# Optimization experiments

Hardware: AMD Instinct MI355X
Metric: run time of the kernel (lower is better)

Reference implementation:

```python
import jax, jax.numpy as jnp
import numpy as np

HEADS = 8
DIM_HEAD = 64
SCALE = DIM_HEAD ** -0.5


def setup_inputs() -> dict:
    key = jax.random.key(0)
    ks = jax.random.split(key, 6)
    B, T, C, H, W = 16, 64, 512, 64, 64
    inner = HEADS * DIM_HEAD  # 512
    return {
        "vision_feature": jax.random.normal(ks[0], (B, C, H, W), jnp.float32),
        "language_feature": jax.random.normal(ks[1], (B, T, C), jnp.float32),
        "mask": jnp.ones((B, T), jnp.int32),  # unused by the module's forward
        "Wq": jax.random.normal(ks[2], (inner, C), jnp.float32) * (C ** -0.5),
        "Wk": jax.random.normal(ks[3], (inner, C), jnp.float32) * (C ** -0.5),
        "Wv": jax.random.normal(ks[4], (inner, C), jnp.float32) * (C ** -0.5),
        "Wo": jax.random.normal(ks[5], (C, inner), jnp.float32) * (inner ** -0.5),
    }


def reference(vision_feature, language_feature, mask, Wq, Wk, Wv, Wo):
    B, T, C = language_feature.shape
    _, _, H, W = vision_feature.shape
    S = H * W
    # 1x1 conv projections == matmuls over the channel dim
    q = jnp.einsum('btc,ic->bti', language_feature, Wq)           # (B, T, inner)
    vis = vision_feature.reshape(B, C, S)                          # (B, C, S)
    k = jnp.einsum('ic,bcs->bis', Wk, vis)                         # (B, inner, S)
    v = jnp.einsum('ic,bcs->bis', Wv, vis)                         # (B, inner, S)
    # split heads: channel index = n*dim_head + d  (n outermost)
    q = q.reshape(B, T, HEADS, DIM_HEAD).transpose(2, 0, 1, 3)     # (h, B, T, d)
    k = k.reshape(B, HEADS, DIM_HEAD, S).transpose(1, 0, 2, 3)     # (h, B, d, S)
    v = v.reshape(B, HEADS, DIM_HEAD, S).transpose(1, 0, 3, 2)     # (h, B, S, d)
    att = jax.nn.softmax(jnp.einsum('hbtd,hbds->hbts', q, k) * SCALE, axis=-1)
    out = jnp.einsum('hbts,hbsd->hbtd', att, v)                    # (h, B, T, d)
    # merge heads back: b (n c) tokens -> equivalently (B, T, h*d)
    out = out.transpose(1, 2, 0, 3).reshape(B, T, HEADS * DIM_HEAD)
    out = jnp.einsum('bti,oi->bto', out, Wo)                       # (B, T, C)
    return out
```

## Files before the change

### kernel.cpp

```cpp
#include <hip/hip_runtime.h>
#include <stdint.h>

typedef __attribute__((ext_vector_type(8))) short short8;
typedef __attribute__((ext_vector_type(4))) short short4v;
typedef __attribute__((ext_vector_type(4))) float float4v;
typedef __attribute__((ext_vector_type(8))) __bf16 bf16x8;

#define NCH 4

__device__ __forceinline__ float4v mfma16x16x32(short8 a, short8 b, float4v c) {
  return __builtin_amdgcn_mfma_f32_16x16x32_bf16(
      __builtin_bit_cast(bf16x8, a), __builtin_bit_cast(bf16x8, b), c, 0, 0, 0);
}

__device__ __forceinline__ short f2bf(float f) {
  uint32_t u = __builtin_bit_cast(uint32_t, f);
  u += 0x7fffu + ((u >> 16) & 1u);
  return (short)(u >> 16);
}

__device__ __forceinline__ float bf2f(short s) {
  return __builtin_bit_cast(float, ((uint32_t)(uint16_t)s) << 16);
}

__device__ __forceinline__ void load_lds16(const short* g, short* l) {
  __builtin_amdgcn_global_load_lds(
      (const __attribute__((address_space(1))) void*)g,
      (__attribute__((address_space(3))) void*)l, 16, 0, 0);
}

__global__ __launch_bounds__(256) void convert5(
    const float* __restrict__ sl, short* __restrict__ dl,
    const float* __restrict__ s1, short* __restrict__ d1,
    const float* __restrict__ s2, short* __restrict__ d2,
    const float* __restrict__ s3, short* __restrict__ d3,
    const float* __restrict__ s4, short* __restrict__ d4) {
  const float* src; short* dst; int n4;
  switch (blockIdx.y) {
    case 0: src = sl; dst = dl; n4 = 131072; break;
    case 1: src = s1; dst = d1; n4 = 65536; break;
    case 2: src = s2; dst = d2; n4 = 65536; break;
    case 3: src = s3; dst = d3; n4 = 65536; break;
    default: src = s4; dst = d4; n4 = 65536; break;
  }
  const int stride = gridDim.x * blockDim.x;
  for (int i = blockIdx.x * blockDim.x + threadIdx.x; i < n4; i += stride) {
    float4v v = *(const float4v*)(src + (long)i * 4);
    short4v o;
#pragma unroll
    for (int r = 0; r < 4; r++) o[r] = f2bf(v[r]);
    *(short4v*)(dst + (long)i * 4) = o;
  }
}

template <int OUT_F32>
__global__ __launch_bounds__(256) void gemm_nt(
    const short* __restrict__ A, const short* __restrict__ B,
    void* __restrict__ C, int K, int ldc, float scale) {
  __shared__ alignas(16) short lA[128 * 32];
  __shared__ alignas(16) short lB[128 * 32];
  const int tid = threadIdx.x;
  const int lane = tid & 63, w = tid >> 6;
  const int quad = lane >> 4, l16 = lane & 15;
  const int wm = w >> 1, wn = w & 1;
  const long m0 = (long)blockIdx.y * 128, n0 = (long)blockIdx.x * 128;

  float4v acc[4][4];
#pragma unroll
  for (int i = 0; i < 4; i++)
#pragma unroll
    for (int j = 0; j < 4; j++) acc[i][j] = (float4v)0.0f;

  const int srow = tid >> 2;
  const int scol = (((tid & 3) ^ ((srow >> 1) & 3))) * 8;

  load_lds16(&A[(m0 + srow) * K + scol], &lA[tid * 8]);
  load_lds16(&A[(m0 + 64 + srow) * K + scol], &lA[2048 + tid * 8]);
  load_lds16(&B[(n0 + srow) * K + scol], &lB[tid * 8]);
  load_lds16(&B[(n0 + 64 + srow) * K + scol], &lB[2048 + tid * 8]);

  for (int kt = 0; kt < K; kt += 32) {
    __syncthreads();

    short8 af[4], bf[4];
#pragma unroll
    for (int t = 0; t < 4; t++) {
      const int ra = wm * 64 + t * 16 + l16;
      const int rb = wn * 64 + t * 16 + l16;
      af[t] = *(const short8*)&lA[ra * 32 + ((quad ^ ((ra >> 1) & 3)) * 8)];
      bf[t] = *(const short8*)&lB[rb * 32 + ((quad ^ ((rb >> 1) & 3)) * 8)];
    }
    __syncthreads();

    if (kt + 32 < K) {
      load_lds16(&A[(m0 + srow) * K + kt + 32 + scol], &lA[tid * 8]);
      load_lds16(&A[(m0 + 64 + srow) * K + kt + 32 + scol], &lA[2048 + tid * 8]);
      load_lds16(&B[(n0 + srow) * K + kt + 32 + scol], &lB[tid * 8]);
      load_lds16(&B[(n0 + 64 + srow) * K + kt + 32 + scol], &lB[2048 + tid * 8]);
    }
#pragma unroll
    for (int i = 0; i < 4; i++)
#pragma unroll
      for (int j = 0; j < 4; j++)
        acc[i][j] = mfma16x16x32(af[i], bf[j], acc[i][j]);
  }

  const int cm = wm * 64 + quad * 4;
  const int cn = wn * 64 + l16;
  if (OUT_F32) {
    float* Cf = (float*)C;
#pragma unroll
    for (int i = 0; i < 4; i++)
#pragma unroll
      for (int j = 0; j < 4; j++) {
        const long gn = n0 + cn + j * 16;
#pragma unroll
        for (int r = 0; r < 4; r++)
          Cf[(m0 + cm + i * 16 + r) * (long)ldc + gn] = acc[i][j][r] * scale;
      }
  } else {
    short* Cs = (short*)C;
#pragma unroll
    for (int i = 0; i < 4; i++)
#pragma unroll
      for (int j = 0; j < 4; j++) {
        const long gn = n0 + cn + j * 16;
#pragma unroll
        for (int r = 0; r < 4; r++)
          Cs[(m0 + cm + i * 16 + r) * (long)ldc + gn] = f2bf(acc[i][j][r] * scale);
      }
  }
}

__global__ __launch_bounds__(512) void gemm_kv(
    const short* __restrict__ Wk, const short* __restrict__ Wv,
    const short* __restrict__ visT, long sV,
    short* __restrict__ kout, short* __restrict__ vout, long sKV) {
  __shared__ alignas(16) short smem[12288];
  short* lWk = smem;
  short* lWv = smem + 4096;
  short* lVis = smem + 8192;
  const int tid = threadIdx.x;
  const int lane = tid & 63, w = tid >> 6;
  const int quad = lane >> 4, l16 = lane & 15;
  const int role = w >> 2;
  const int wq = w & 3, wm = wq >> 1, wn = wq & 1;
  const long n0 = (long)blockIdx.x * 128;
  const long m0 = (long)blockIdx.y * 128;
  const short* vis = visT + blockIdx.z * sV;
  short* kz = kout + blockIdx.z * sKV;
  short* vz = vout + blockIdx.z * sKV;

  float4v acc[4][4];
#pragma unroll
  for (int i = 0; i < 4; i++)
#pragma unroll
    for (int j = 0; j < 4; j++) acc[i][j] = (float4v)0.0f;

  const int srow = tid >> 2;
  const int scol = (((tid & 3) ^ ((srow >> 1) & 3))) * 8;
  const short* lW = role ? lWv : lWk;

  load_lds16(&Wk[(m0 + srow) * 512 + scol], &lWk[tid * 8]);
  load_lds16(&Wv[(m0 + srow) * 512 + scol], &lWv[tid * 8]);
  load_lds16(&vis[(n0 + srow) * 512 + scol], &lVis[tid * 8]);

  for (int kt = 0; kt < 512; kt += 32) {
    __syncthreads();

    short8 af[4], bf[4];
#pragma unroll
    for (int t = 0; t < 4; t++) {
      const int ra = wm * 64 + t * 16 + l16;
      const int rb = wn * 64 + t * 16 + l16;
      af[t] = *(const short8*)&lW[ra * 32 + ((quad ^ ((ra >> 1) & 3)) * 8)];
      bf[t] = *(const short8*)&lVis[rb * 32 + ((quad ^ ((rb >> 1) & 3)) * 8)];
    }
    __syncthreads();

    if (kt + 32 < 512) {
      load_lds16(&Wk[(m0 + srow) * 512 + kt + 32 + scol], &lWk[tid * 8]);
      load_lds16(&Wv[(m0 + srow) * 512 + kt + 32 + scol], &lWv[tid * 8]);
      load_lds16(&vis[(n0 + srow) * 512 + kt + 32 + scol], &lVis[tid * 8]);
    }
#pragma unroll
    for (int i = 0; i < 4; i++)
#pragma unroll
      for (int j = 0; j < 4; j++)
        acc[i][j] = mfma16x16x32(af[i], bf[j], acc[i][j]);
  }

  const int cm = wm * 64 + quad * 4;
  const int cn = wn * 64 + l16;

  if (role == 1) {
#pragma unroll
    for (int i = 0; i < 4; i++)
#pragma unroll
      for (int j = 0; j < 4; j++) {
        const long gn = n0 + cn + j * 16;
#pragma unroll
        for (int r = 0; r < 4; r++)
          vz[(m0 + cm + i * 16 + r) * 4096 + gn] = f2bf(acc[i][j][r]);
      }
  }

  short* scratch = smem;
#pragma unroll
  for (int h = 0; h < 2; h++) {
    __syncthreads();
    if (role == 0 && wn == h) {
#pragma unroll
      for (int j = 0; j < 4; j++)
#pragma unroll
        for (int i = 0; i < 4; i++) {
          const int nloc = j * 16 + l16;
          const int m = wm * 64 + i * 16 + quad * 4;
          short4v pk;
#pragma unroll
          for (int r = 0; r < 4; r++) pk[r] = f2bf(acc[i][j][r]);
          *(short4v*)&scratch[nloc * 136 + m] = pk;
        }
    }
    __syncthreads();
    {
      const int row = tid >> 3;
      const int off = (tid & 7) * 16;
      short8 v0 = *(const short8*)&scratch[row * 136 + off];
      short8 v1 = *(const short8*)&scratch[row * 136 + off + 8];
      *(short8*)&kz[(n0 + h * 64 + row) * 512 + m0 + off] = v0;
      *(short8*)&kz[(n0 + h * 64 + row) * 512 + m0 + off + 8] = v1;
    }
  }
}

__global__ __launch_bounds__(256) void transpose_f2b(
    const float* __restrict__ vis, short* __restrict__ visT) {
  __shared__ alignas(16) short buf[64][68];
  const int tid = threadIdx.x;
  const long bz = blockIdx.z;
  const long s0 = (long)blockIdx.x * 64;
  const long c0 = (long)blockIdx.y * 64;
  const float* src = vis + bz * 512 * 4096;
  short* dst = visT + bz * 4096 * 512;
  const int tr = tid >> 4;
  const int tc4 = (tid & 15) * 4;
#pragma unroll
  for (int i = 0; i < 4; i++) {
    const int c = tr + i * 16;
    float4v val = *(const float4v*)&src[(c0 + c) * 4096 + s0 + tc4];
    buf[tc4 + 0][c] = f2bf(val[0]);
    buf[tc4 + 1][c] = f2bf(val[1]);
    buf[tc4 + 2][c] = f2bf(val[2]);
    buf[tc4 + 3][c] = f2bf(val[3]);
  }
  __syncthreads();
#pragma unroll
  for (int i = 0; i < 4; i++) {
    const int s = tr + i * 16;
    short4v val = *(const short4v*)&buf[s][tc4];
    *(short4v*)&dst[(s0 + s) * 512 + c0 + tc4] = val;
  }
}

__global__ __launch_bounds__(256) void attn_part(
    const short* __restrict__ q, const short* __restrict__ kws,
    const short* __restrict__ vws, float* __restrict__ Opart,
    float* __restrict__ lpart, int b0) {
  const int h = blockIdx.x;
  const int bz = blockIdx.y;
  const int ch = blockIdx.z;
  const int tid = threadIdx.x;
  const int lane = tid & 63, w = tid >> 6;
  const int quad = lane >> 4, l16 = lane & 15;

  __shared__ alignas(16) short lq[64 * 64];
  __shared__ alignas(16) short lk[128 * 64];
  __shared__ alignas(16) short lv[64 * 128];
  __shared__ alignas(16) short lp[64 * 128];
  __shared__ float lsum[64];

  const short* qb = q + ((long)(b0 + bz) * 64) * 512 + h * 64;
  const short* kb = kws + (long)bz * 4096 * 512 + h * 64;
  const short* vb = vws + (long)bz * 512 * 4096 + (long)h * 64 * 4096;

  if (tid < 64) lsum[tid] = 0.0f;
  {
    const int qr = tid >> 3;
    const int qc = ((tid & 7) ^ (qr & 7)) * 8;
    load_lds16(&qb[qr * 512 + qc], &lq[tid * 8]);
    load_lds16(&qb[(32 + qr) * 512 + qc], &lq[2048 + tid * 8]);
  }
  const int s0_first = ch * (4096 / NCH);
  const int send = s0_first + (4096 / NCH);
#pragma unroll
  for (int it = 0; it < 4; it++) {
    const int li = tid + it * 256;
    const int kr = li >> 3;
    const int kc = ((li & 7) ^ (kr & 7)) * 8;
    load_lds16(&kb[(long)(s0_first + kr) * 512 + kc], &lk[li * 8]);
  }
#pragma unroll
  for (int it = 0; it < 4; it++) {
    const int li = tid + it * 256;
    const int vr = li >> 4;
    const int vc = ((li & 15) ^ (vr & 7)) * 8;
    load_lds16(&vb[(long)vr * 4096 + s0_first + vc], &lv[li * 8]);
  }
  __syncthreads();

  short8 aq[4][2];
#pragma unroll
  for (int mt = 0; mt < 4; mt++)
#pragma unroll
    for (int ks = 0; ks < 2; ks++) {
      const int ra = mt * 16 + l16;
      aq[mt][ks] = *(const short8*)&lq[ra * 64 + (((ks * 4 + quad) ^ (ra & 7)) * 8)];
    }

  float4v osc[4];
#pragma unroll
  for (int mt = 0; mt < 4; mt++) osc[mt] = (float4v)0.0f;
  float lrow[4][4] = {};

  for (int s0 = s0_first; s0 < send; s0 += 128) {
    short8 bk[2][2];
#pragma unroll
    for (int ks = 0; ks < 2; ks++)
#pragma unroll
      for (int jn = 0; jn < 2; jn++) {
        const int rb = (2 * w + jn) * 16 + l16;
        bk[ks][jn] = *(const short8*)&lk[rb * 64 + (((ks * 4 + quad) ^ (rb & 7)) * 8)];
      }
    short8 bv[4];
#pragma unroll
    for (int ks = 0; ks < 4; ks++) {
      const int rv = w * 16 + l16;
      bv[ks] = *(const short8*)&lv[rv * 128 + (((ks * 4 + quad) ^ (rv & 7)) * 8)];
    }
    __syncthreads();

    if (s0 + 128 < send) {
#pragma unroll
      for (int it = 0; it < 4; it++) {
        const int li = tid + it * 256;
        const int kr = li >> 3;
        const int kc = ((li & 7) ^ (kr & 7)) * 8;
        load_lds16(&kb[(long)(s0 + 128 + kr) * 512 + kc], &lk[li * 8]);
      }
#pragma unroll
      for (int it = 0; it < 4; it++) {
        const int li = tid + it * 256;
        const int vr = li >> 4;
        const int vc = ((li & 15) ^ (vr & 7)) * 8;
        load_lds16(&vb[(long)vr * 4096 + s0 + 128 + vc], &lv[li * 8]);
      }
    }

    float4v sc[4][2];
#pragma unroll
    for (int mt = 0; mt < 4; mt++)
#pragma unroll
      for (int jn = 0; jn < 2; jn++) sc[mt][jn] = (float4v)0.0f;
#pragma unroll
    for (int ks = 0; ks < 2; ks++)
#pragma unroll
      for (int mt = 0; mt < 4; mt++)
#pragma unroll
        for (int jn = 0; jn < 2; jn++)
          sc[mt][jn] = mfma16x16x32(aq[mt][ks], bk[ks][jn], sc[mt][jn]);

#pragma unroll
    for (int mt = 0; mt < 4; mt++)
#pragma unroll
      for (int jn = 0; jn < 2; jn++)
#pragma unroll
        for (int r = 0; r < 4; r++) {
          const float scv = fminf(fmaxf(sc[mt][jn][r], -80.0f), 30.0f);
          const short sp = f2bf(__expf(scv));
          lrow[mt][r] += bf2f(sp);
          const int rowp = mt * 16 + quad * 4 + r;
          const int col = (2 * w + jn) * 16 + l16;
          lp[rowp * 128 + (((col >> 3) ^ (rowp & 7)) * 8) + (col & 7)] = sp;
        }
    __syncthreads();

#pragma unroll
    for (int ks = 0; ks < 4; ks++)
#pragma unroll
      for (int mt = 0; mt < 4; mt++) {
        const int rp = mt * 16 + l16;
        const short8 ap = *(const short8*)&lp[rp * 128 + (((ks * 4 + quad) ^ (rp & 7)) * 8)];
        osc[mt] = mfma16x16x32(ap, bv[ks], osc[mt]);
      }
    __syncthreads();
  }

#pragma unroll
  for (int mt = 0; mt < 4; mt++)
#pragma unroll
    for (int r = 0; r < 4; r++) {
      float v = lrow[mt][r];
      v += __shfl_xor(v, 1);
      v += __shfl_xor(v, 2);
      v += __shfl_xor(v, 4);
      v += __shfl_xor(v, 8);
      if (l16 == 0) atomicAdd(&lsum[mt * 16 + quad * 4 + r], v);
    }
  __syncthreads();

  const long bh = bz * 8 + h;
  float* op = Opart + ((bh * NCH + ch) * 64) * 64 + w * 16 + l16;
#pragma unroll
  for (int mt = 0; mt < 4; mt++)
#pragma unroll
    for (int r = 0; r < 4; r++)
      op[(long)(mt * 16 + quad * 4 + r) * 64] = osc[mt][r];
  if (tid < 64) lpart[(bh * NCH + ch) * 64 + tid] = lsum[tid];
}

__global__ __launch_bounds__(256) void attn_combine(
    const float* __restrict__ Opart, const float* __restrict__ lpart,
    short* __restrict__ tmp, int b0, int nbh) {
  const int total = nbh * 4096;
  for (int idx = blockIdx.x * 256 + threadIdx.x; idx < total;
       idx += gridDim.x * 256) {
    const int bh = idx >> 12;
    const int td = idx & 4095;
    const int t = td >> 6, d = td & 63;
    float o = 0.0f, l = 0.0f;
#pragma unroll
    for (int c = 0; c < NCH; c++) {
      o += Opart[((long)bh * NCH + c) * 4096 + td];
      l += lpart[(bh * NCH + c) * 64 + t];
    }
    const int b = b0 + (bh >> 3), h = bh & 7;
    tmp[((long)b * 64 + t) * 512 + h * 64 + d] = f2bf(o / l);
  }
}

extern "C" void kernel_launch(void* const* d_in, const int* in_sizes, int n_in,
                              void* d_out, int out_size, void* d_ws, size_t ws_size,
                              hipStream_t stream) {
  (void)in_sizes; (void)n_in; (void)out_size;
  const float* vis = (const float*)d_in[0];
  const float* lang = (const float*)d_in[1];
  const float* Wq = (const float*)d_in[3];
  const float* Wk = (const float*)d_in[4];
  const float* Wv = (const float*)d_in[5];
  const float* Wo = (const float*)d_in[6];
  float* out = (float*)d_out;

  char* ws = (char*)d_ws;
  const size_t MB = 1 << 20;
  short* q_ws = (short*)(ws + 0 * MB);
  short* tmp_ws = (short*)(ws + 1 * MB);
  short* langb = (short*)(ws + 2 * MB);
  short* Wqb = (short*)(ws + 3 * MB);
  short* Wkb = (short*)(ws + 3 * MB + 512 * 1024);
  short* Wvb = (short*)(ws + 4 * MB);
  short* Wob = (short*)(ws + 4 * MB + 512 * 1024);
  char* grp = ws + 5 * MB;

  const long batch_elems = 4096l * 512;
  int g = 16;
  const int cands[5] = {1, 2, 4, 8, 16};
  for (int ci = 0; ci < 5; ci++) {
    const size_t need = 5 * MB + 3ull * (16 / cands[ci]) * batch_elems * 2;
    if (need <= ws_size) { g = cands[ci]; break; }
  }
  const int Bg = 16 / g;
  short* visT = (short*)grp;
  short* k_ws = visT + (long)Bg * batch_elems;
  short* v_ws = k_ws + (long)Bg * batch_elems;
  float* Opart = (float*)visT;
  float* lptr = Opart + (long)Bg * 8 * NCH * 4096;

  convert5<<<dim3(128, 5), 256, 0, stream>>>(lang, langb, Wq, Wqb, Wk, Wkb,
                                             Wv, Wvb, Wo, Wob);

  gemm_nt<0><<<dim3(4, 8), 256, 0, stream>>>(langb, Wqb, q_ws, 512, 512, 0.125f);

  for (int gi = 0; gi < g; gi++) {
    const int b0 = gi * Bg;
    transpose_f2b<<<dim3(64, 8, Bg), 256, 0, stream>>>(vis + (long)b0 * batch_elems, visT);
    gemm_kv<<<dim3(32, 4, Bg), 512, 0, stream>>>(Wkb, Wvb, visT, batch_elems,
                                                 k_ws, v_ws, batch_elems);
    attn_part<<<dim3(8, Bg, NCH), 256, 0, stream>>>(q_ws, k_ws, v_ws, Opart, lptr, b0);
    attn_combine<<<512, 256, 0, stream>>>(Opart, lptr, tmp_ws, b0, Bg * 8);
  }

  gemm_nt<1><<<dim3(4, 8), 256, 0, stream>>>(tmp_ws, Wob, out, 512, 512, 1.0f);
}
```

Measured before the change: 379.7 us.

## Fuse fp32-to-bf16 vision transpose into separate K and V projection kernels

Removes the standalone transpose/convert kernel and the bf16 visT buffer: new proj_kv kernels read fp32 vision features directly, convert to bf16 in registers, stage them in double-buffered LDS, and keep the full 32-row weight slab resident. K and V are now computed by two launches with a smaller 32x128 tile, so the vision input is read from global memory twice and the weight tile is less reused. The attention split count NCH is also doubled, and the workspace layout gives Opart its own region instead of aliasing visT.

```diff
diff --git a/kernel.cpp b/kernel.cpp
--- a/kernel.cpp
+++ b/kernel.cpp
@@ -6,7 +6,7 @@
 typedef __attribute__((ext_vector_type(4))) float float4v;
 typedef __attribute__((ext_vector_type(8))) __bf16 bf16x8;
 
-#define NCH 4
+#define NCH 8
 
 __device__ __forceinline__ float4v mfma16x16x32(short8 a, short8 b, float4v c) {
   return __builtin_amdgcn_mfma_f32_16x16x32_bf16(
@@ -132,134 +132,109 @@
   }
 }
 
-__global__ __launch_bounds__(512) void gemm_kv(
-    const short* __restrict__ Wk, const short* __restrict__ Wv,
-    const short* __restrict__ visT, long sV,
-    short* __restrict__ kout, short* __restrict__ vout, long sKV) {
-  __shared__ alignas(16) short smem[12288];
-  short* lWk = smem;
-  short* lWv = smem + 4096;
-  short* lVis = smem + 8192;
+template <int TRANS>
+__global__ __launch_bounds__(256) void proj_kv(
+    const short* __restrict__ W, const float* __restrict__ vis,
+    short* __restrict__ out) {
+  __shared__ alignas(16) short lW[32 * 512];
+  __shared__ alignas(16) short lV[2][4376];
   const int tid = threadIdx.x;
   const int lane = tid & 63, w = tid >> 6;
   const int quad = lane >> 4, l16 = lane & 15;
-  const int role = w >> 2;
-  const int wq = w & 3, wm = wq >> 1, wn = wq & 1;
-  const long n0 = (long)blockIdx.x * 128;
-  const long m0 = (long)blockIdx.y * 128;
-  const short* vis = visT + blockIdx.z * sV;
-  short* kz = kout + blockIdx.z * sKV;
-  short* vz = vout + blockIdx.z * sKV;
-
-  float4v acc[4][4];
-#pragma unroll
-  for (int i = 0; i < 4; i++)
-#pragma unroll
-    for (int j = 0; j < 4; j++) acc[i][j] = (float4v)0.0f;
-
-  const int srow = tid >> 2;
-  const int scol = (((tid & 3) ^ ((srow >> 1) & 3))) * 8;
-  const short* lW = role ? lWv : lWk;
-
-  load_lds16(&Wk[(m0 + srow) * 512 + scol], &lWk[tid * 8]);
-  load_lds16(&Wv[(m0 + srow) * 512 + scol], &lWv[tid * 8]);
-  load_lds16(&vis[(n0 + srow) * 512 + scol], &lVis[tid * 8]);
-
-  for (int kt = 0; kt < 512; kt += 32) {
-    __syncthreads();
-
-    short8 af[4], bf[4];
-#pragma unroll
-    for (int t = 0; t < 4; t++) {
-      const int ra = wm * 64 + t * 16 + l16;
-      const int rb = wn * 64 + t * 16 + l16;
-      af[t] = *(const short8*)&lW[ra * 32 + ((quad ^ ((ra >> 1) & 3)) * 8)];
-      bf[t] = *(const short8*)&lVis[rb * 32 + ((quad ^ ((rb >> 1) & 3)) * 8)];
-    }
-    __syncthreads();
-
-    if (kt + 32 < 512) {
-      load_lds16(&Wk[(m0 + srow) * 512 + kt + 32 + scol], &lWk[tid * 8]);
-      load_lds16(&Wv[(m0 + srow) * 512 + kt + 32 + scol], &lWv[tid * 8]);
-      load_lds16(&vis[(n0 + srow) * 512 + kt + 32 + scol], &lVis[tid * 8]);
-    }
-#pragma unroll
-    for (int i = 0; i < 4; i++)
-#pragma unroll
-      for (int j = 0; j < 4; j++)
-        acc[i][j] = mfma16x16x32(af[i], bf[j], acc[i][j]);
-  }
-
-  const int cm = wm * 64 + quad * 4;
-  const int cn = wn * 64 + l16;
-
-  if (role == 1) {
-#pragma unroll
-    for (int i = 0; i < 4; i++)
-#pragma unroll
-      for (int j = 0; j < 4; j++) {
-        const long gn = n0 + cn + j * 16;
+  const int m0 = blockIdx.x * 32;
+  const long n0 = (long)blockIdx.y * 128;
+  const long b = blockIdx.z;
+  const float* vb = vis + (b * 512) * 4096 + n0;
+
+#pragma unroll
+  for (int r = 0; r < 8; r++) {
+    const int row = w + 4 * r;
+    load_lds16(&W[(m0 + row) * 512 + ((lane ^ (row & 7)) * 8)],
+               &lW[row * 512 + lane * 8]);
+  }
+
+  const int vc = w * 8 + (lane >> 3);
+  const int vs = (lane & 7) * 16;
+  const int vofs = vc * 136 + (vc >> 3) * 8 + vs;
+
+  float4v rg[2][4];
+#pragma unroll
+  for (int p = 0; p < 2; p++) {
+    const float* src = vb + (long)(p * 32 + vc) * 4096 + vs;
+#pragma unroll
+    for (int q = 0; q < 4; q++) rg[p][q] = ((const float4v*)src)[q];
+  }
+
+  float4v acc[2][2];
+#pragma unroll
+  for (int i = 0; i < 2; i++)
+#pragma unroll
+    for (int j = 0; j < 2; j++) acc[i][j] = (float4v)0.0f;
+
+  for (int kt = 0, it = 0; kt < 512; kt += 32, it++) {
+    const int pb = it & 1;
+    short8 c0, c1;
+#pragma unroll
+    for (int j = 0; j < 4; j++) {
+      c0[j] = f2bf(rg[pb][0][j]);
+      c0[4 + j] = f2bf(rg[pb][1][j]);
+      c1[j] = f2bf(rg[pb][2][j]);
+      c1[4 + j] = f2bf(rg[pb][3][j]);
+    }
+    *(short8*)&lV[pb][vofs] = c0;
+    *(short8*)&lV[pb][vofs + 8] = c1;
+    __syncthreads();
+
+    if (kt + 64 < 512) {
+      const float* src = vb + (long)(kt + 64 + vc) * 4096 + vs;
+#pragma unroll
+      for (int q = 0; q < 4; q++) rg[pb][q] = ((const float4v*)src)[q];
+    }
+
+    short8 af[2];
+#pragma unroll
+    for (int mt = 0; mt < 2; mt++) {
+      const int ra = mt * 16 + l16;
+      af[mt] = *(const short8*)&lW[ra * 512 + ((((kt >> 3) + quad) ^ (ra & 7)) * 8)];
+    }
+    short8 bf[2];
+#pragma unroll
+    for (int nt = 0; nt < 2; nt++) {
+      const int sb = w * 32 + nt * 16 + l16;
+#pragma unroll
+      for (int j = 0; j < 8; j++) {
+        const int c = quad * 8 + j;
+        bf[nt][j] = lV[pb][c * 136 + (c >> 3) * 8 + sb];
+      }
+    }
+#pragma unroll
+    for (int mt = 0; mt < 2; mt++)
+#pragma unroll
+      for (int nt = 0; nt < 2; nt++)
+        acc[mt][nt] = mfma16x16x32(af[mt], bf[nt], acc[mt][nt]);
+  }
+
+  if (TRANS) {
+#pragma unroll
+    for (int mt = 0; mt < 2; mt++)
+#pragma unroll
+      for (int nt = 0; nt < 2; nt++) {
+        const long s = n0 + w * 32 + nt * 16 + l16;
+        short4v pk;
+#pragma unroll
+        for (int r = 0; r < 4; r++) pk[r] = f2bf(acc[mt][nt][r]);
+        *(short4v*)&out[(b * 4096 + s) * 512 + m0 + mt * 16 + quad * 4] = pk;
+      }
+  } else {
+#pragma unroll
+    for (int mt = 0; mt < 2; mt++)
+#pragma unroll
+      for (int nt = 0; nt < 2; nt++) {
+        const long s = n0 + w * 32 + nt * 16 + l16;
 #pragma unroll
         for (int r = 0; r < 4; r++)
-          vz[(m0 + cm + i * 16 + r) * 4096 + gn] = f2bf(acc[i][j][r]);
-      }
-  }
-
-  short* scratch = smem;
-#pragma unroll
-  for (int h = 0; h < 2; h++) {
-    __syncthreads();
-    if (role == 0 && wn == h) {
-#pragma unroll
-      for (int j = 0; j < 4; j++)
-#pragma unroll
-        for (int i = 0; i < 4; i++) {
-          const int nloc = j * 16 + l16;
-          const int m = wm * 64 + i * 16 + quad * 4;
-          short4v pk;
-#pragma unroll
-          for (int r = 0; r < 4; r++) pk[r] = f2bf(acc[i][j][r]);
-          *(short4v*)&scratch[nloc * 136 + m] = pk;
-        }
-    }
-    __syncthreads();
-    {
-      const int row = tid >> 3;
-      const int off = (tid & 7) * 16;
-      short8 v0 = *(const short8*)&scratch[row * 136 + off];
-      short8 v1 = *(const short8*)&scratch[row * 136 + off + 8];
-      *(short8*)&kz[(n0 + h * 64 + row) * 512 + m0 + off] = v0;
-      *(short8*)&kz[(n0 + h * 64 + row) * 512 + m0 + off + 8] = v1;
-    }
-  }
-}
-
-__global__ __launch_bounds__(256) void transpose_f2b(
-    const float* __restrict__ vis, short* __restrict__ visT) {
-  __shared__ alignas(16) short buf[64][68];
-  const int tid = threadIdx.x;
-  const long bz = blockIdx.z;
-  const long s0 = (long)blockIdx.x * 64;
-  const long c0 = (long)blockIdx.y * 64;
-  const float* src = vis + bz * 512 * 4096;
-  short* dst = visT + bz * 4096 * 512;
-  const int tr = tid >> 4;
-  const int tc4 = (tid & 15) * 4;
-#pragma unroll
-  for (int i = 0; i < 4; i++) {
-    const int c = tr + i * 16;
-    float4v val = *(const float4v*)&src[(c0 + c) * 4096 + s0 + tc4];
-    buf[tc4 + 0][c] = f2bf(val[0]);
-    buf[tc4 + 1][c] = f2bf(val[1]);
-    buf[tc4 + 2][c] = f2bf(val[2]);
-    buf[tc4 + 3][c] = f2bf(val[3]);
-  }
-  __syncthreads();
-#pragma unroll
-  for (int i = 0; i < 4; i++) {
-    const int s = tr + i * 16;
-    short4v val = *(const short4v*)&buf[s][tc4];
-    *(short4v*)&dst[(s0 + s) * 512 + c0 + tc4] = val;
+          out[(b * 512 + m0 + mt * 16 + quad * 4 + r) * 4096 + s] = f2bf(acc[mt][nt][r]);
+      }
   }
 }
 
@@ -466,14 +441,15 @@
   int g = 16;
   const int cands[5] = {1, 2, 4, 8, 16};
   for (int ci = 0; ci < 5; ci++) {
-    const size_t need = 5 * MB + 3ull * (16 / cands[ci]) * batch_elems * 2;
+    const int Bgc = 16 / cands[ci];
+    const size_t need = 5 * MB + 2ull * Bgc * batch_elems * 2
+                        + (size_t)Bgc * 8 * NCH * 4096 * 4 + (1 * MB);
     if (need <= ws_size) { g = cands[ci]; break; }
   }
   const int Bg = 16 / g;
-  short* visT = (short*)grp;
-  short* k_ws = visT + (long)Bg * batch_elems;
+  short* k_ws = (short*)grp;
   short* v_ws = k_ws + (long)Bg * batch_elems;
-  float* Opart = (float*)visT;
+  float* Opart = (float*)(v_ws + (long)Bg * batch_elems);
   float* lptr = Opart + (long)Bg * 8 * NCH * 4096;
 
   convert5<<<dim3(128, 5), 256, 0, stream>>>(lang, langb, Wq, Wqb, Wk, Wkb,
@@ -483,9 +459,9 @@
 
   for (int gi = 0; gi < g; gi++) {
     const int b0 = gi * Bg;
-    transpose_f2b<<<dim3(64, 8, Bg), 256, 0, stream>>>(vis + (long)b0 * batch_elems, visT);
-    gemm_kv<<<dim3(32, 4, Bg), 512, 0, stream>>>(Wkb, Wvb, visT, batch_elems,
-                                                 k_ws, v_ws, batch_elems);
+    const float* visg = vis + (long)b0 * 512 * 4096;
+    proj_kv<1><<<dim3(16, 32, Bg), 256, 0, stream>>>(Wkb, visg, k_ws);
+    proj_kv<0><<<dim3(16, 32, Bg), 256, 0, stream>>>(Wvb, visg, v_ws);
     attn_part<<<dim3(8, Bg, NCH), 256, 0, stream>>>(q_ws, k_ws, v_ws, Opart, lptr, b0);
     attn_combine<<<512, 256, 0, stream>>>(Opart, lptr, tmp_ws, b0, Bg * 8);
   }
```

New measurement: 592.8 us. 56.1% more time.
